# Optimization experiments

Measured on AMD Instinct MI355X. Metric: run time of the kernel, lower is better.

## Reference

```python
import jax, jax.numpy as jnp
import numpy as np

N, T, D, H = 32, 1024, 1152, 16
DH = D // H            # 72
MLP = int(D * 4.0)     # 4608
EPS = 1e-6


def setup_inputs() -> dict:
    key = jax.random.key(0)
    ks = jax.random.split(key, 14)
    s = 0.02
    return {
        "x": jax.random.normal(ks[0], (N, T, D), jnp.float32),
        "c": jax.random.normal(ks[1], (N, D), jnp.float32),
        "qkv_w": jax.random.normal(ks[2], (D, 3 * D), jnp.float32) * s,
        "qkv_b": jax.random.normal(ks[3], (3 * D,), jnp.float32) * s,
        "proj_w": jax.random.normal(ks[4], (D, D), jnp.float32) * s,
        "proj_b": jax.random.normal(ks[5], (D,), jnp.float32) * s,
        "fc1_w": jax.random.normal(ks[6], (D, MLP), jnp.float32) * s,
        "fc1_b": jax.random.normal(ks[7], (MLP,), jnp.float32) * s,
        "fc2_w": jax.random.normal(ks[8], (MLP, D), jnp.float32) * s,
        "fc2_b": jax.random.normal(ks[9], (D,), jnp.float32) * s,
        "ada_w": jax.random.normal(ks[10], (D, 6 * D), jnp.float32) * s,
        "ada_b": jax.random.normal(ks[11], (6 * D,), jnp.float32) * s,
    }


def _layernorm(x):
    m = jnp.mean(x, axis=-1, keepdims=True)
    v = jnp.var(x, axis=-1, keepdims=True)
    return (x - m) * jax.lax.rsqrt(v + EPS)


def _modulate(x, shift, scale):
    # shift, scale: (N, D) broadcast over T
    return x * (1.0 + scale[:, None, :]) + shift[:, None, :]


def _attention(x, qkv_w, qkv_b, proj_w, proj_b):
    n, t, d = x.shape
    scale = DH ** (-0.5)
    qkv = x @ qkv_w + qkv_b                       # (N,T,3D)
    qkv = qkv.reshape(n, t, 3, H, DH)
    q, k, v = qkv[:, :, 0], qkv[:, :, 1], qkv[:, :, 2]  # each (N,T,H,DH)
    # Faithful to source: matmul over the LAST two dims -> per-token
    # head-vs-head attention of shape (N,T,H,H), softmax over heads.
    attn = jnp.einsum("nthd,ntkd->nthk", q * scale, k)
    attn = jax.nn.softmax(attn, axis=-1)
    out = jnp.einsum("nthk,ntkd->nthd", attn, v)  # (N,T,H,DH)
    out = out.transpose(0, 2, 1, 3).reshape(n, t, d)  # faithful scramble
    return out @ proj_w + proj_b


def _mlp(x, fc1_w, fc1_b, fc2_w, fc2_b):
    h = jax.nn.gelu(x @ fc1_w + fc1_b, approximate=False)  # exact GELU (torch default)
    return h @ fc2_w + fc2_b


def reference(x, c, qkv_w, qkv_b, proj_w, proj_b, fc1_w, fc1_b, fc2_w, fc2_b,
              ada_w, ada_b):
    ada = jax.nn.silu(c) @ ada_w + ada_b          # (N, 6D)
    (shift_msa, scale_msa, gate_msa,
     shift_mlp, scale_mlp, gate_mlp) = jnp.split(ada, 6, axis=1)
    x = x + gate_msa[:, None, :] * _attention(
        _modulate(_layernorm(x), shift_msa, scale_msa),
        qkv_w, qkv_b, proj_w, proj_b)
    x = x + gate_mlp[:, None, :] * _mlp(
        _modulate(_layernorm(x), shift_mlp, scale_mlp),
        fc1_w, fc1_b, fc2_w, fc2_b)
    return x
```

## Files before the change

kernel.cpp:

```cpp
#include <hip/hip_runtime.h>

#define DEV __device__ __forceinline__

typedef __attribute__((ext_vector_type(8))) short short8;
typedef __attribute__((ext_vector_type(8))) __bf16 bf16x8;
typedef __attribute__((ext_vector_type(4))) float f32x4;

#define TD      1024
#define DD      1152
#define DHH     72
#define MLPD    4608
#define QKVN    3456
#define ADAN    6912
#define MROWS   32768

DEV unsigned short f32_to_bf16(float f) {
  unsigned int u = __float_as_uint(f);
  u += 0x7fffu + ((u >> 16) & 1u);
  return (unsigned short)(u >> 16);
}

DEV void gl16(const void* g, void* l) {
  __builtin_amdgcn_global_load_lds((__attribute__((address_space(1))) void*)g,
                                   (__attribute__((address_space(3))) void*)l,
                                   16, 0, 0);
}

DEV bf16x8 zero_bf16x8() {
  short8 z = {0, 0, 0, 0, 0, 0, 0, 0};
  return __builtin_bit_cast(bf16x8, z);
}

DEV float gelu_exact(float v) {
  return 0.5f * v * (1.0f + erff(v * 0.70710678118654752f));
}

#define WAITV(n) asm volatile("s_waitcnt vmcnt(" #n ")" ::: "memory")

__global__ __launch_bounds__(256) void wtrans_kernel(const float* __restrict__ W,
                                                     unsigned short* __restrict__ Wt,
                                                     int K, int N) {
  __shared__ unsigned short tile[32][33];
  const int nb = blockIdx.x * 32, kb = blockIdx.y * 32;
  const int tx = threadIdx.x, ty = threadIdx.y;
  #pragma unroll
  for (int i = ty; i < 32; i += 8)
    tile[i][tx] = f32_to_bf16(W[(size_t)(kb + i) * N + nb + tx]);
  __syncthreads();
  #pragma unroll
  for (int i = ty; i < 32; i += 8)
    Wt[(size_t)(nb + i) * K + kb + tx] = tile[tx][i];
}

__global__ __launch_bounds__(256) void ada_kernel(const float* __restrict__ c,
                                                  const float* __restrict__ ada_w,
                                                  const float* __restrict__ ada_b,
                                                  float* __restrict__ ada_out) {
  __shared__ float sc[DD];
  const int n = blockIdx.y;
  const int col = blockIdx.x * 256 + threadIdx.x;
  for (int i = threadIdx.x; i < DD; i += 256) {
    float v = c[(size_t)n * DD + i];
    sc[i] = v / (1.0f + __expf(-v));
  }
  __syncthreads();
  float acc = ada_b[col];
  #pragma unroll 8
  for (int k = 0; k < DD; ++k)
    acc += sc[k] * ada_w[(size_t)k * ADAN + col];
  ada_out[(size_t)n * ADAN + col] = acc;
}

__global__ __launch_bounds__(256) void ln_mod_kernel(const float* __restrict__ X,
                                                     const float* __restrict__ ada,
                                                     int soff,
                                                     unsigned short* __restrict__ out) {
  const int row = blockIdx.x;
  const int batch = row >> 10;
  const float* xr = X + (size_t)row * DD;
  const int t = threadIdx.x;

  float4 v0 = reinterpret_cast<const float4*>(xr)[t];
  float4 v1 = make_float4(0.f, 0.f, 0.f, 0.f);
  const bool has2 = (t < 32);
  if (has2) v1 = reinterpret_cast<const float4*>(xr)[256 + t];

  float s  = v0.x + v0.y + v0.z + v0.w + v1.x + v1.y + v1.z + v1.w;
  float sq = v0.x*v0.x + v0.y*v0.y + v0.z*v0.z + v0.w*v0.w
           + v1.x*v1.x + v1.y*v1.y + v1.z*v1.z + v1.w*v1.w;
  #pragma unroll
  for (int m = 1; m < 64; m <<= 1) {
    s  += __shfl_xor(s, m);
    sq += __shfl_xor(sq, m);
  }
  __shared__ float red[8];
  const int wv = t >> 6;
  if ((t & 63) == 0) { red[wv] = s; red[4 + wv] = sq; }
  __syncthreads();
  s  = red[0] + red[1] + red[2] + red[3];
  sq = red[4] + red[5] + red[6] + red[7];
  const float mean = s * (1.0f / 1152.0f);
  const float var  = sq * (1.0f / 1152.0f) - mean * mean;
  const float rstd = rsqrtf(var + 1e-6f);

  const float* shp = ada + (size_t)batch * ADAN + soff;
  const float* scp = shp + DD;
  unsigned short* orow = out + (size_t)row * DD;

  {
    const int col = t * 4;
    ushort4 o4;
    o4.x = f32_to_bf16((v0.x - mean) * rstd * (1.0f + scp[col + 0]) + shp[col + 0]);
    o4.y = f32_to_bf16((v0.y - mean) * rstd * (1.0f + scp[col + 1]) + shp[col + 1]);
    o4.z = f32_to_bf16((v0.z - mean) * rstd * (1.0f + scp[col + 2]) + shp[col + 2]);
    o4.w = f32_to_bf16((v0.w - mean) * rstd * (1.0f + scp[col + 3]) + shp[col + 3]);
    reinterpret_cast<ushort4*>(orow)[t] = o4;
  }
  if (has2) {
    const int col = 1024 + t * 4;
    ushort4 o4;
    o4.x = f32_to_bf16((v1.x - mean) * rstd * (1.0f + scp[col + 0]) + shp[col + 0]);
    o4.y = f32_to_bf16((v1.y - mean) * rstd * (1.0f + scp[col + 1]) + shp[col + 1]);
    o4.z = f32_to_bf16((v1.z - mean) * rstd * (1.0f + scp[col + 2]) + shp[col + 2]);
    o4.w = f32_to_bf16((v1.w - mean) * rstd * (1.0f + scp[col + 3]) + shp[col + 3]);
    reinterpret_cast<ushort4*>(orow)[256 + t] = o4;
  }
}

template <int EPI>
__global__ __launch_bounds__(256) void gemm2b(
    const unsigned short* __restrict__ A, const unsigned short* __restrict__ Bt,
    const float* __restrict__ bias, const float* __restrict__ ada, int ada_off,
    const float* __restrict__ resid, unsigned short* __restrict__ out_bf,
    float* __restrict__ out_f, int N, int K, int ntn) {
  __shared__ unsigned short lds[32768];
  const int tid = threadIdx.x;
  const int lane = tid & 63, w = tid >> 6;
  const int wm = w >> 1, wn = w & 1;
  const int l15 = lane & 15, lg = lane >> 4;

  const int nwg = 256 * ntn, cpx = nwg >> 3;
  const int wg = (blockIdx.x & 7) * cpx + (blockIdx.x >> 3);
  const int bm = wg / ntn, bn = wg - bm * ntn;

  const unsigned short* __restrict__ Ag = A + (size_t)bm * 128 * K;
  const unsigned short* __restrict__ Bg = Bt + (size_t)bn * 128 * K;

  const int srow = tid >> 3;
  const int ch0 = ((tid & 7) ^ (srow & 7)) * 8;

#define STG(BUFB, KT) do {                                                               \
    _Pragma("unroll") for (int r_ = 0; r_ < 4; ++r_)                                     \
      gl16(Ag + (size_t)(srow + r_ * 32) * K + (size_t)(KT) * 64 + ch0,                  \
           &lds[(BUFB) + r_ * 2048 + tid * 8]);                                          \
    _Pragma("unroll") for (int r_ = 0; r_ < 4; ++r_)                                     \
      gl16(Bg + (size_t)(srow + r_ * 32) * K + (size_t)(KT) * 64 + ch0,                  \
           &lds[(BUFB) + 8192 + r_ * 2048 + tid * 8]);                                   \
  } while (0)

  const int chA0 = (lg ^ (l15 & 7)) * 8;
  const int chA1 = chA0 ^ 32;
  const int arow0 = wm * 64 + l15;
  const int brow0 = wn * 64 + l15;

  f32x4 acc[4][4];
  #pragma unroll
  for (int m = 0; m < 4; ++m)
    #pragma unroll
    for (int nn = 0; nn < 4; ++nn)
      acc[m][nn] = (f32x4){0.f, 0.f, 0.f, 0.f};

  const int NT = K >> 6;

  STG(0, 0);

  for (int t = 0; t < NT; ++t) {
    const int cb = (t & 1) << 14, nb = cb ^ 16384;
    const unsigned short* lb = lds + cb;
    if (t + 1 < NT) {
      STG(nb, t + 1);
      WAITV(8);
    } else {
      WAITV(0);
    }
    __builtin_amdgcn_s_barrier();

    bf16x8 a0[4], b0[4], a1[4], b1[4];
    #pragma unroll
    for (int mf = 0; mf < 4; ++mf) a0[mf] = *(const bf16x8*)&lb[(arow0 + mf * 16) * 64 + chA0];
    #pragma unroll
    for (int nf = 0; nf < 4; ++nf) b0[nf] = *(const bf16x8*)&lb[8192 + (brow0 + nf * 16) * 64 + chA0];
    __builtin_amdgcn_s_setprio(1);
    #pragma unroll
    for (int mf = 0; mf < 4; ++mf)
      #pragma unroll
      for (int nf = 0; nf < 4; ++nf)
        acc[mf][nf] = __builtin_amdgcn_mfma_f32_16x16x32_bf16(a0[mf], b0[nf], acc[mf][nf], 0, 0, 0);
    __builtin_amdgcn_s_setprio(0);
    #pragma unroll
    for (int mf = 0; mf < 4; ++mf) a1[mf] = *(const bf16x8*)&lb[(arow0 + mf * 16) * 64 + chA1];
    #pragma unroll
    for (int nf = 0; nf < 4; ++nf) b1[nf] = *(const bf16x8*)&lb[8192 + (brow0 + nf * 16) * 64 + chA1];
    __builtin_amdgcn_s_setprio(1);
    #pragma unroll
    for (int mf = 0; mf < 4; ++mf)
      #pragma unroll
      for (int nf = 0; nf < 4; ++nf)
        acc[mf][nf] = __builtin_amdgcn_mfma_f32_16x16x32_bf16(a1[mf], b1[nf], acc[mf][nf], 0, 0, 0);
    __builtin_amdgcn_s_setprio(0);
    __builtin_amdgcn_s_barrier();
  }
#undef STG

  const int batch = bm >> 3;
  const size_t row0 = (size_t)bm * 128 + wm * 64;
  const int col0 = bn * 128 + wn * 64;
  #pragma unroll
  for (int nf = 0; nf < 4; ++nf) {
    const int colg = col0 + nf * 16 + l15;
    const float bv = bias[colg];
    float g2 = 0.0f;
    if constexpr (EPI == 1 || EPI == 3) g2 = ada[(size_t)batch * ADAN + ada_off + colg];
    #pragma unroll
    for (int mf = 0; mf < 4; ++mf) {
      #pragma unroll
      for (int r = 0; r < 4; ++r) {
        const size_t idx = (row0 + mf * 16 + lg * 4 + r) * (size_t)N + colg;
        const float v = acc[mf][nf][r] + bv;
        if constexpr (EPI == 0)      out_bf[idx] = f32_to_bf16(v);
        else if constexpr (EPI == 2) out_bf[idx] = f32_to_bf16(gelu_exact(v));
        else if constexpr (EPI == 1) out_f[idx] = resid[idx] + g2 * v;
        else                         out_f[idx] = out_f[idx] + g2 * v;
      }
    }
  }
}

__global__ __launch_bounds__(256) void attn_kernel(const unsigned short* __restrict__ qkv,
                                                   unsigned short* __restrict__ y) {
  const int tid = threadIdx.x, w = tid >> 6, lane = tid & 63;
  const int l15 = lane & 15, lg = lane >> 4;
  const int tok = blockIdx.x * 4 + w;
  const int n = tok >> 10, t = tok & 1023;

  __shared__ unsigned short Pl[4][16 * 32];
  __shared__ unsigned short Vl[4][16 * 80];

  for (int i = lane; i < 16 * 32; i += 64)
    if ((i & 31) >= 16) Pl[w][i] = 0;

  const size_t rowb = (size_t)tok * QKVN;
  const float scale = 0.11785113019775793f;

  bf16x8 aq[3];
  #pragma unroll
  for (int kk = 0; kk < 3; ++kk) {
    const int d0 = kk * 32 + lg * 8;
    aq[kk] = (d0 < DHH) ? *(const bf16x8*)&qkv[rowb + l15 * DHH + d0] : zero_bf16x8();
  }

  for (int c = lane; c < 144; c += 64) {
    const int r = c / 9, cc = (c % 9) * 8;
    *(short8*)&Vl[w][r * 80 + cc] = *(const short8*)&qkv[rowb + 2 * DD + r * DHH + cc];
  }

  f32x4 s = (f32x4){0.f, 0.f, 0.f, 0.f};
  #pragma unroll
  for (int kk = 0; kk < 3; ++kk) {
    const int d0 = kk * 32 + lg * 8;
    bf16x8 bk = (d0 < DHH) ? *(const bf16x8*)&qkv[rowb + DD + l15 * DHH + d0] : zero_bf16x8();
    s = __builtin_amdgcn_mfma_f32_16x16x32_bf16(aq[kk], bk, s, 0, 0, 0);
  }

  float p[4], mx[4], ssum[4];
  #pragma unroll
  for (int r = 0; r < 4; ++r) { p[r] = s[r] * scale; mx[r] = p[r]; }
  #pragma unroll
  for (int mk = 1; mk <= 8; mk <<= 1)
    #pragma unroll
    for (int r = 0; r < 4; ++r) mx[r] = fmaxf(mx[r], __shfl_xor(mx[r], mk));
  #pragma unroll
  for (int r = 0; r < 4; ++r) { p[r] = __expf(p[r] - mx[r]); ssum[r] = p[r]; }
  #pragma unroll
  for (int mk = 1; mk <= 8; mk <<= 1)
    #pragma unroll
    for (int r = 0; r < 4; ++r) ssum[r] += __shfl_xor(ssum[r], mk);

  #pragma unroll
  for (int r = 0; r < 4; ++r)
    Pl[w][(lg * 4 + r) * 32 + l15] = f32_to_bf16(p[r] / ssum[r]);

  bf16x8 pa = *(const bf16x8*)&Pl[w][l15 * 32 + lg * 8];
  const int kb = (lg & 1) * 8;
  f32x4 o[5];
  #pragma unroll
  for (int df = 0; df < 5; ++df) {
    short8 bvv;
    #pragma unroll
    for (int j = 0; j < 8; ++j)
      bvv[j] = (short)Vl[w][(kb + j) * 80 + df * 16 + l15];
    o[df] = __builtin_amdgcn_mfma_f32_16x16x32_bf16(
        pa, __builtin_bit_cast(bf16x8, bvv), (f32x4){0.f, 0.f, 0.f, 0.f}, 0, 0, 0);
  }

  unsigned short* yb = y + (size_t)n * (TD * DD);
  #pragma unroll
  for (int df = 0; df < 5; ++df) {
    const int d = df * 16 + l15;
    if (d < DHH) {
      #pragma unroll
      for (int r = 0; r < 4; ++r) {
        const int h = lg * 4 + r;
        yb[h * 73728 + t * DHH + d] = f32_to_bf16(o[df][r]);
      }
    }
  }
}

extern "C" void kernel_launch(void* const* d_in, const int* in_sizes, int n_in,
                              void* d_out, int out_size, void* d_ws, size_t ws_size,
                              hipStream_t stream) {
  (void)in_sizes; (void)n_in; (void)out_size; (void)ws_size;
  const float* x      = (const float*)d_in[0];
  const float* c      = (const float*)d_in[1];
  const float* qkv_w  = (const float*)d_in[2];
  const float* qkv_b  = (const float*)d_in[3];
  const float* proj_w = (const float*)d_in[4];
  const float* proj_b = (const float*)d_in[5];
  const float* fc1_w  = (const float*)d_in[6];
  const float* fc1_b  = (const float*)d_in[7];
  const float* fc2_w  = (const float*)d_in[8];
  const float* fc2_b  = (const float*)d_in[9];
  const float* ada_w  = (const float*)d_in[10];
  const float* ada_b  = (const float*)d_in[11];
  float* out = (float*)d_out;

  char* ws = (char*)d_ws;
  unsigned short* hbuf    = (unsigned short*)ws;
  unsigned short* qkvbuf  = hbuf;
  unsigned short* attnbuf = hbuf + (size_t)MROWS * QKVN;
  size_t off = 301989888ull;
  unsigned short* xm    = (unsigned short*)(ws + off); off += 75497472ull;
  unsigned short* wtq   = (unsigned short*)(ws + off); off += (size_t)QKVN * DD * 2;
  unsigned short* wtp   = (unsigned short*)(ws + off); off += (size_t)DD * DD * 2;
  unsigned short* wtf1  = (unsigned short*)(ws + off); off += (size_t)MLPD * DD * 2;
  unsigned short* wtf2  = (unsigned short*)(ws + off); off += (size_t)DD * MLPD * 2;
  float*          adab  = (float*)(ws + off); off += 884736ull;

  const dim3 tb(32, 8);
  hipLaunchKernelGGL(wtrans_kernel, dim3(QKVN / 32, DD / 32), tb, 0, stream, qkv_w, wtq, DD, QKVN);
  hipLaunchKernelGGL(wtrans_kernel, dim3(DD / 32, DD / 32),   tb, 0, stream, proj_w, wtp, DD, DD);
  hipLaunchKernelGGL(wtrans_kernel, dim3(MLPD / 32, DD / 32), tb, 0, stream, fc1_w, wtf1, DD, MLPD);
  hipLaunchKernelGGL(wtrans_kernel, dim3(DD / 32, MLPD / 32), tb, 0, stream, fc2_w, wtf2, MLPD, DD);

  hipLaunchKernelGGL(ada_kernel, dim3(ADAN / 256, 32), dim3(256), 0, stream, c, ada_w, ada_b, adab);

  hipLaunchKernelGGL(ln_mod_kernel, dim3(MROWS), dim3(256), 0, stream, x, adab, 0, xm);

  hipLaunchKernelGGL((gemm2b<0>), dim3(256 * 27), dim3(256), 0, stream,
                     xm, wtq, qkv_b, nullptr, 0, nullptr, qkvbuf, nullptr, QKVN, DD, 27);

  hipLaunchKernelGGL(attn_kernel, dim3(MROWS / 4), dim3(256), 0, stream, qkvbuf, attnbuf);

  hipLaunchKernelGGL((gemm2b<1>), dim3(256 * 9), dim3(256), 0, stream,
                     attnbuf, wtp, proj_b, adab, 2304, x, nullptr, out, DD, DD, 9);

  hipLaunchKernelGGL(ln_mod_kernel, dim3(MROWS), dim3(256), 0, stream, out, adab, 3456, xm);

  hipLaunchKernelGGL((gemm2b<2>), dim3(256 * 36), dim3(256), 0, stream,
                     xm, wtf1, fc1_b, nullptr, 0, nullptr, hbuf, nullptr, MLPD, DD, 36);

  hipLaunchKernelGGL((gemm2b<3>), dim3(256 * 9), dim3(256), 0, stream,
                     hbuf, wtf2, fc2_b, adab, 5760, nullptr, nullptr, out, DD, MLPD, 9);
}
```

Baseline: 1.812 ms.

## Switch GEMMs to 256x128 tiles with 8 waves and BK=32 staging

```diff
diff --git a/kernel.cpp b/kernel.cpp
--- a/kernel.cpp
+++ b/kernel.cpp
@@ -128,38 +128,36 @@
 }
 
 template <int EPI>
-__global__ __launch_bounds__(256) void gemm2b(
+__global__ __launch_bounds__(512) void gemm3b(
     const unsigned short* __restrict__ A, const unsigned short* __restrict__ Bt,
     const float* __restrict__ bias, const float* __restrict__ ada, int ada_off,
     const float* __restrict__ resid, unsigned short* __restrict__ out_bf,
     float* __restrict__ out_f, int N, int K, int ntn) {
-  __shared__ unsigned short lds[32768];
+  __shared__ unsigned short lds[24576];
   const int tid = threadIdx.x;
   const int lane = tid & 63, w = tid >> 6;
   const int wm = w >> 1, wn = w & 1;
   const int l15 = lane & 15, lg = lane >> 4;
 
-  const int nwg = 256 * ntn, cpx = nwg >> 3;
+  const int nwg = 128 * ntn, cpx = nwg >> 3;
   const int wg = (blockIdx.x & 7) * cpx + (blockIdx.x >> 3);
   const int bm = wg / ntn, bn = wg - bm * ntn;
 
-  const unsigned short* __restrict__ Ag = A + (size_t)bm * 128 * K;
+  const unsigned short* __restrict__ Ag = A + (size_t)bm * 256 * K;
   const unsigned short* __restrict__ Bg = Bt + (size_t)bn * 128 * K;
 
-  const int srow = tid >> 3;
-  const int ch0 = ((tid & 7) ^ (srow & 7)) * 8;
-
-#define STG(BUFB, KT) do {                                                               \
-    _Pragma("unroll") for (int r_ = 0; r_ < 4; ++r_)                                     \
-      gl16(Ag + (size_t)(srow + r_ * 32) * K + (size_t)(KT) * 64 + ch0,                  \
-           &lds[(BUFB) + r_ * 2048 + tid * 8]);                                          \
-    _Pragma("unroll") for (int r_ = 0; r_ < 4; ++r_)                                     \
-      gl16(Bg + (size_t)(srow + r_ * 32) * K + (size_t)(KT) * 64 + ch0,                  \
-           &lds[(BUFB) + 8192 + r_ * 2048 + tid * 8]);                                   \
+  const int srow = tid >> 2;
+  const int gch = ((tid & 3) ^ ((tid >> 3) & 3)) * 8;
+
+#define STG(SL, KT) do {                                                                 \
+    gl16(Ag + (size_t)srow * K + (size_t)(KT) * 32 + gch, &lds[(SL) + tid * 8]);         \
+    gl16(Ag + (size_t)(srow + 128) * K + (size_t)(KT) * 32 + gch,                        \
+         &lds[(SL) + 4096 + tid * 8]);                                                   \
+    gl16(Bg + (size_t)srow * K + (size_t)(KT) * 32 + gch,                                \
+         &lds[(SL) + 8192 + tid * 8]);                                                   \
   } while (0)
 
-  const int chA0 = (lg ^ (l15 & 7)) * 8;
-  const int chA1 = chA0 ^ 32;
+  const int chA = (lg ^ ((l15 >> 1) & 3)) * 8;
   const int arow0 = wm * 64 + l15;
   const int brow0 = wn * 64 + l15;
 
@@ -170,50 +168,40 @@
     for (int nn = 0; nn < 4; ++nn)
       acc[m][nn] = (f32x4){0.f, 0.f, 0.f, 0.f};
 
-  const int NT = K >> 6;
+  const int NT = K >> 5;
 
   STG(0, 0);
-
   for (int t = 0; t < NT; ++t) {
-    const int cb = (t & 1) << 14, nb = cb ^ 16384;
-    const unsigned short* lb = lds + cb;
+    const int sl = (t & 1) * 12288, ns = sl ^ 12288;
     if (t + 1 < NT) {
-      STG(nb, t + 1);
-      WAITV(8);
+      STG(ns, t + 1);
+      WAITV(3);
     } else {
       WAITV(0);
     }
     __builtin_amdgcn_s_barrier();
 
-    bf16x8 a0[4], b0[4], a1[4], b1[4];
-    #pragma unroll
-    for (int mf = 0; mf < 4; ++mf) a0[mf] = *(const bf16x8*)&lb[(arow0 + mf * 16) * 64 + chA0];
-    #pragma unroll
-    for (int nf = 0; nf < 4; ++nf) b0[nf] = *(const bf16x8*)&lb[8192 + (brow0 + nf * 16) * 64 + chA0];
+    const unsigned short* lb = lds + sl;
+    bf16x8 af[4], bfv[4];
+    #pragma unroll
+    for (int mf = 0; mf < 4; ++mf)
+      af[mf] = *(const bf16x8*)&lb[(arow0 + mf * 16) * 32 + chA];
+    #pragma unroll
+    for (int nf = 0; nf < 4; ++nf)
+      bfv[nf] = *(const bf16x8*)&lb[8192 + (brow0 + nf * 16) * 32 + chA];
     __builtin_amdgcn_s_setprio(1);
     #pragma unroll
     for (int mf = 0; mf < 4; ++mf)
       #pragma unroll
       for (int nf = 0; nf < 4; ++nf)
-        acc[mf][nf] = __builtin_amdgcn_mfma_f32_16x16x32_bf16(a0[mf], b0[nf], acc[mf][nf], 0, 0, 0);
-    __builtin_amdgcn_s_setprio(0);
-    #pragma unroll
-    for (int mf = 0; mf < 4; ++mf) a1[mf] = *(const bf16x8*)&lb[(arow0 + mf * 16) * 64 + chA1];
-    #pragma unroll
-    for (int nf = 0; nf < 4; ++nf) b1[nf] = *(const bf16x8*)&lb[8192 + (brow0 + nf * 16) * 64 + chA1];
-    __builtin_amdgcn_s_setprio(1);
-    #pragma unroll
-    for (int mf = 0; mf < 4; ++mf)
-      #pragma unroll
-      for (int nf = 0; nf < 4; ++nf)
-        acc[mf][nf] = __builtin_amdgcn_mfma_f32_16x16x32_bf16(a1[mf], b1[nf], acc[mf][nf], 0, 0, 0);
+        acc[mf][nf] = __builtin_amdgcn_mfma_f32_16x16x32_bf16(af[mf], bfv[nf], acc[mf][nf], 0, 0, 0);
     __builtin_amdgcn_s_setprio(0);
     __builtin_amdgcn_s_barrier();
   }
 #undef STG
 
-  const int batch = bm >> 3;
-  const size_t row0 = (size_t)bm * 128 + wm * 64;
+  const int batch = bm >> 2;
+  const size_t row0 = (size_t)bm * 256 + wm * 64;
   const int col0 = bn * 128 + wn * 64;
   #pragma unroll
   for (int nf = 0; nf < 4; ++nf) {
@@ -357,19 +345,19 @@
 
   hipLaunchKernelGGL(ln_mod_kernel, dim3(MROWS), dim3(256), 0, stream, x, adab, 0, xm);
 
-  hipLaunchKernelGGL((gemm2b<0>), dim3(256 * 27), dim3(256), 0, stream,
+  hipLaunchKernelGGL((gemm3b<0>), dim3(128 * 27), dim3(512), 0, stream,
                      xm, wtq, qkv_b, nullptr, 0, nullptr, qkvbuf, nullptr, QKVN, DD, 27);
 
   hipLaunchKernelGGL(attn_kernel, dim3(MROWS / 4), dim3(256), 0, stream, qkvbuf, attnbuf);
 
-  hipLaunchKernelGGL((gemm2b<1>), dim3(256 * 9), dim3(256), 0, stream,
+  hipLaunchKernelGGL((gemm3b<1>), dim3(128 * 9), dim3(512), 0, stream,
                      attnbuf, wtp, proj_b, adab, 2304, x, nullptr, out, DD, DD, 9);
 
   hipLaunchKernelGGL(ln_mod_kernel, dim3(MROWS), dim3(256), 0, stream, out, adab, 3456, xm);
 
-  hipLaunchKernelGGL((gemm2b<2>), dim3(256 * 36), dim3(256), 0, stream,
+  hipLaunchKernelGGL((gemm3b<2>), dim3(128 * 36), dim3(512), 0, stream,
                      xm, wtf1, fc1_b, nullptr, 0, nullptr, hbuf, nullptr, MLPD, DD, 36);
 
-  hipLaunchKernelGGL((gemm2b<3>), dim3(256 * 9), dim3(256), 0, stream,
+  hipLaunchKernelGGL((gemm3b<3>), dim3(128 * 9), dim3(512), 0, stream,
                      hbuf, wtf2, fc2_b, adab, 5760, nullptr, nullptr, out, DD, MLPD, 9);
 }
```

New measurement: 1.755 ms. 3.1% less time.
